# Optimization experiments

Measured on AMD Instinct MI355X. Metric: run time of the kernel, lower is better.

The kernel has to match this reference:

```python
import jax, jax.numpy as jnp
import numpy as np

EPS = 1e-08


def setup_inputs() -> dict:
    key = jax.random.key(0)
    B, D = 8192, 512
    student_output = jax.random.normal(key, (B, D), dtype=jnp.float32)
    return {"student_output": student_output}


def reference(student_output) -> jnp.ndarray:
    # F.normalize(p=2, dim=-1, eps=EPS): x / max(||x||, eps)
    norm = jnp.linalg.norm(student_output, axis=-1, keepdims=True)
    x = student_output / jnp.maximum(norm, EPS)

    n = x.shape[0]
    # Pairwise inner products; mask the diagonal with -1 (self-match)
    dots = jnp.matmul(x, x.T)  # [B, B]
    idx = jnp.arange(n)
    dots = dots.at[idx, idx].set(-1.0)
    I = jnp.argmax(dots, axis=1)  # nearest neighbor index per row

    # torch.nn.PairwiseDistance(2, eps): ||x1 - x2 + eps||_2
    diff = x - x[I] + EPS
    distances = jnp.linalg.norm(diff, axis=-1)  # [B]
    loss = -jnp.mean(jnp.log(distances + EPS))
    return loss
```

## Files before the change

kernel.cpp:

```cpp
#include <hip/hip_runtime.h>
#include <hip/hip_bf16.h>
#include <math.h>

#define D_DIM 512
#define TM    128
#define TN    256

typedef int i32x4 __attribute__((ext_vector_type(4)));
typedef unsigned long long u64;


__device__ inline void async16(unsigned char* lds, const unsigned char* g) {
    __builtin_amdgcn_global_load_lds(
        (const __attribute__((address_space(1))) void*)g,
        (__attribute__((address_space(3))) void*)lds,
        16, 0, 0);
}

__device__ inline bool decode_tile(int l, int& bi, int& bj) {
    const int x    = l & 7;
    const int rank = l >> 3;
    if (rank >= 132) return false;
    const int L0 = 2 * x + 2;
    if (rank < L0)              { bj = x;      bi = rank; }
    else if (rank < 66)         { bj = 31 - x; bi = rank - L0; }
    else if (rank < 2 * x + 84) { bj = x + 8;  bi = rank - 66; }
    else                        { bj = 23 - x; bi = rank - (2 * x + 84); }
    return true;
}


__global__ __launch_bounds__(256) void normalize_rows(
        const float* __restrict__ in, unsigned char* __restrict__ xb,
        float* __restrict__ inv_norm, u64* __restrict__ best,
        float* __restrict__ acc, int* __restrict__ cnt) {
    const int row  = blockIdx.x * 4 + (threadIdx.x >> 6);
    const int lane = threadIdx.x & 63;
    if (blockIdx.x == 0 && threadIdx.x == 0) { acc[0] = 0.f; cnt[0] = 0; }
    const float4* rp = (const float4*)(in + (size_t)row * D_DIM) + lane * 2;
    float4 a = rp[0], b = rp[1];
    float s = a.x*a.x + a.y*a.y + a.z*a.z + a.w*a.w
            + b.x*b.x + b.y*b.y + b.z*b.z + b.w*b.w;
    #pragma unroll
    for (int m = 1; m <= 32; m <<= 1) s += __shfl_xor(s, m, 64);
    float inv = 1.0f / fmaxf(sqrtf(s), 1e-8f);
    if (lane == 0) {
        inv_norm[row] = inv;
        best[row] = 0ull;
    }
    float sc = inv * 127.0f;
    int q0 = __float2int_rn(a.x*sc), q1 = __float2int_rn(a.y*sc);
    int q2 = __float2int_rn(a.z*sc), q3 = __float2int_rn(a.w*sc);
    int q4 = __float2int_rn(b.x*sc), q5 = __float2int_rn(b.y*sc);
    int q6 = __float2int_rn(b.z*sc), q7 = __float2int_rn(b.w*sc);
    int lo = (q0 & 255) | ((q1 & 255) << 8) | ((q2 & 255) << 16) | ((q3 & 255) << 24);
    int hi = (q4 & 255) | ((q5 & 255) << 8) | ((q6 & 255) << 16) | ((q7 & 255) << 24);
    ((int2*)(xb + (size_t)row * D_DIM))[lane] = make_int2(lo, hi);
}


__global__ __launch_bounds__(512, 4) void gemm_argmax(
        const unsigned char* __restrict__ X, u64* __restrict__ best) {
    __shared__ unsigned char smem[73728];
    __shared__ unsigned ready[8];
    __shared__ unsigned readdone[8];
    unsigned char* As0 = smem;
    unsigned char* Bs0 = smem + 24576;
    unsigned int* rmerge = (unsigned int*)smem;
    unsigned int* cmerge = (unsigned int*)(smem + 2048);

    int bi, bj;
    if (!decode_tile(blockIdx.x, bi, bj)) return;
    const int m0 = bi * TM;
    const int n0 = bj * TN;

    const int t    = threadIdx.x;
    const int lane = t & 63;
    const int w    = t >> 6;
    const int wm   = w >> 2;
    const int wn   = w & 3;
    const int qr   = lane & 15;
    const int quad = lane >> 4;

    const int srcsl = ((t & 3) ^ ((t >> 3) & 3)) * 16;
    const unsigned char* gA  = X + (size_t)(m0 + (t >> 2)) * D_DIM + srcsl;
    const unsigned char* gB  = X + (size_t)(n0 + (t >> 2)) * D_DIM + srcsl;
    const unsigned char* gB2 = gB + (size_t)128 * D_DIM;

    if (t < 8)  ready[t] = 0;
    if (t >= 8 && t < 16) readdone[t - 8] = 0;
    __syncthreads();

    i32x4 accm[4][4];
    #pragma unroll
    for (int mi = 0; mi < 4; mi++)
        #pragma unroll
        for (int ni = 0; ni < 4; ni++)
            accm[mi][ni] = (i32x4){0, 0, 0, 0};

    const int rdsl = (quad ^ ((qr >> 1) & 3)) * 16;

    #define STAGE(buf, k0)                                            \
        do {                                                          \
            async16(As0 + (buf) * 8192 + t * 16,         gA + (k0));  \
            async16(Bs0 + (buf) * 16384 + t * 16,        gB + (k0));  \
            async16(Bs0 + (buf) * 16384 + 8192 + t * 16, gB2 + (k0)); \
        } while (0)

    #define SPIN(p, v)                                                \
        while (*(volatile unsigned*)(p) < (v)) __builtin_amdgcn_s_sleep(2)

    STAGE(0, 0);
    STAGE(1, 64);

    #pragma unroll
    for (int t8 = 0; t8 < 8; t8++) {
        const int cur = t8 % 3;
        if (t8 >= 1 && t8 < 6) SPIN(&readdone[t8 - 1], 8u);
        if (t8 < 6) STAGE((t8 + 2) % 3, (t8 + 2) * 64);
        if (t8 < 6)      { asm volatile("s_waitcnt vmcnt(6)" ::: "memory"); }
        else if (t8 == 6){ asm volatile("s_waitcnt vmcnt(3)" ::: "memory"); }
        else             { asm volatile("s_waitcnt vmcnt(0)" ::: "memory"); }
        if (lane == 0) atomicAdd(&ready[t8], 1u);
        SPIN(&ready[t8], 8u);

        i32x4 av[4], bv[4];
        const unsigned char* pA = As0 + cur * 8192  + (wm * 64 + qr) * 64 + rdsl;
        const unsigned char* pB = Bs0 + cur * 16384 + (wn * 64 + qr) * 64 + rdsl;
        #pragma unroll
        for (int mi = 0; mi < 4; mi++)
            av[mi] = *(const i32x4*)(pA + mi * 1024);
        #pragma unroll
        for (int ni = 0; ni < 4; ni++)
            bv[ni] = *(const i32x4*)(pB + ni * 1024);
        asm volatile("s_waitcnt lgkmcnt(0)" ::: "memory");
        if (lane == 0) atomicAdd(&readdone[t8], 1u);

        #pragma unroll
        for (int mi = 0; mi < 4; mi++)
            #pragma unroll
            for (int ni = 0; ni < 4; ni++)
                accm[mi][ni] = __builtin_amdgcn_mfma_i32_16x16x64_i8(
                    av[mi], bv[ni], accm[mi][ni], 0, 0, 0);
    }
    #undef STAGE
    #undef SPIN

    const int colg_base = n0 + wn * 64 + qr;

    #pragma unroll
    for (int mi = 0; mi < 4; mi++) {
        #pragma unroll
        for (int r = 0; r < 4; r++) {
            const int rowl = wm * 64 + mi * 16 + quad * 4 + r;
            const int rowg = m0 + rowl;
            unsigned key = 0u;
            #pragma unroll
            for (int ni = 0; ni < 4; ni++) {
                const int colg = colg_base + ni * 16;
                const unsigned lcol = (unsigned)(wn * 64 + ni * 16 + qr);
                unsigned k = (((unsigned)accm[mi][ni][r] + 0x800000u) << 8)
                           | (255u - lcol);
                k = (colg == rowg) ? 0u : k;
                key = key > k ? key : k;
            }
            #pragma unroll
            for (int m = 1; m <= 8; m <<= 1) {
                unsigned o = (unsigned)__shfl_xor((int)key, m, 64);
                key = key > o ? key : o;
            }
            if (qr == 0) rmerge[rowl * 4 + wn] = key;
        }
    }

    #pragma unroll
    for (int ni = 0; ni < 4; ni++) {
        const int colg = colg_base + ni * 16;
        unsigned key = 0u;
        #pragma unroll
        for (int mi = 0; mi < 4; mi++) {
            #pragma unroll
            for (int r = 0; r < 4; r++) {
                const unsigned lrow = (unsigned)(wm * 64 + mi * 16 + quad * 4 + r);
                const int rowg = m0 + (int)lrow;
                unsigned k = (((unsigned)accm[mi][ni][r] + 0x800000u) << 8)
                           | (255u - lrow);
                k = (rowg == colg) ? 0u : k;
                key = key > k ? key : k;
            }
        }
        unsigned o = (unsigned)__shfl_xor((int)key, 16, 64);
        key = key > o ? key : o;
        o = (unsigned)__shfl_xor((int)key, 32, 64);
        key = key > o ? key : o;
        if (quad == 0) cmerge[(wn * 64 + ni * 16 + qr) * 2 + wm] = key;
    }
    __syncthreads();

    if (t < TM) {
        unsigned a0 = rmerge[t * 4], a1 = rmerge[t * 4 + 1];
        unsigned a2 = rmerge[t * 4 + 2], a3 = rmerge[t * 4 + 3];
        unsigned k01 = a0 > a1 ? a0 : a1;
        unsigned k23 = a2 > a3 ? a2 : a3;
        unsigned k = k01 > k23 ? k01 : k23;
        unsigned bd32 = (k >> 8) + 0x7F800000u;
        unsigned colg = (unsigned)(n0 + 255) - (k & 255u);
        u64 kk = ((u64)bd32 << 32) | (u64)(0xFFFFFFFFu - colg);
        atomicMax(&best[m0 + t], kk);
    }
    if (t < TN) {
        unsigned c0 = cmerge[t * 2], c1 = cmerge[t * 2 + 1];
        unsigned k = c0 > c1 ? c0 : c1;
        unsigned bd32 = (k >> 8) + 0x7F800000u;
        unsigned rowg = (unsigned)(m0 + 255) - (k & 255u);
        u64 kk = ((u64)bd32 << 32) | (u64)(0xFFFFFFFFu - rowg);
        atomicMax(&best[n0 + t], kk);
    }
}


__global__ __launch_bounds__(256) void neighbor_reduce(
        const float* __restrict__ in, const float* __restrict__ inv_norm,
        const u64* __restrict__ best, float* __restrict__ acc,
        int* __restrict__ cnt, float* __restrict__ out, int B) {
    const int wave = threadIdx.x >> 6;
    const int lane = threadIdx.x & 63;
    float lsum = 0.f;
    #pragma unroll
    for (int rr = 0; rr < 8; rr++) {
        const int row = blockIdx.x * 32 + wave * 8 + rr;
        u64 k   = best[row];
        int nbr = (int)(0xFFFFFFFFu - (unsigned)(k & 0xFFFFFFFFull));
        float ir  = inv_norm[row];
        float inb = inv_norm[nbr];
        const float4* rp = (const float4*)(in + (size_t)row * D_DIM) + lane * 2;
        const float4* np = (const float4*)(in + (size_t)nbr * D_DIM) + lane * 2;
        float4 r0 = rp[0], r1 = rp[1], q0 = np[0], q1 = np[1];
        float d0 = r0.x*ir - q0.x*inb + 1e-8f, d1 = r0.y*ir - q0.y*inb + 1e-8f;
        float d2 = r0.z*ir - q0.z*inb + 1e-8f, d3 = r0.w*ir - q0.w*inb + 1e-8f;
        float d4 = r1.x*ir - q1.x*inb + 1e-8f, d5 = r1.y*ir - q1.y*inb + 1e-8f;
        float d6 = r1.z*ir - q1.z*inb + 1e-8f, d7 = r1.w*ir - q1.w*inb + 1e-8f;
        float s = d0*d0 + d1*d1 + d2*d2 + d3*d3 + d4*d4 + d5*d5 + d6*d6 + d7*d7;
        #pragma unroll
        for (int m = 1; m <= 32; m <<= 1) s += __shfl_xor(s, m, 64);
        if (lane == 0) lsum += logf(sqrtf(s) + 1e-8f);
    }
    __shared__ float sb[4];
    if (lane == 0) sb[wave] = lsum;
    __syncthreads();
    if (threadIdx.x == 0) {
        float partial = sb[0] + sb[1] + sb[2] + sb[3];
        atomicAdd(acc, partial);
        __threadfence();
        int done = atomicAdd(cnt, 1);
        if (done == gridDim.x - 1) {
            __threadfence();
            float tot = atomicAdd(acc, 0.0f);
            out[0] = -tot / (float)B;
        }
    }
}


extern "C" void kernel_launch(void* const* d_in, const int* in_sizes, int n_in,
                              void* d_out, int out_size, void* d_ws, size_t ws_size,
                              hipStream_t stream) {
    const float* in = (const float*)d_in[0];
    const int B = in_sizes[0] / D_DIM;
    const int nblk = 144 * 8;

    char* w = (char*)d_ws;
    unsigned char* xb = (unsigned char*)w;
    float* invn = (float*)(w + (size_t)B * D_DIM);
    u64*   best = (u64*)(w + (size_t)B * D_DIM + (size_t)B * 4);
    float* acc  = (float*)(w + (size_t)B * D_DIM + (size_t)B * 4 + (size_t)B * 8);
    int*   cnt  = (int*)(acc + 1);
    float* out  = (float*)d_out;

    normalize_rows<<<B / 4, 256, 0, stream>>>(in, xb, invn, best, acc, cnt);
    gemm_argmax<<<nblk, 512, 0, stream>>>(xb, best);
    neighbor_reduce<<<B / 32, 256, 0, stream>>>(in, invn, best, acc, cnt, out, B);
}
```

Baseline: 113.2 us.

## Replace triple-buffered spin-synced pipeline with single-buffer barrier loop for higher occupancy

Drops the three-stage LDS ring buffer and its atomic-counter spin synchronization in favor of a single staging buffer guarded by __syncthreads each K step. The launch bound is raised to allow more resident blocks per CU, relying on inter-block occupancy instead of intra-block prefetch to hide global load latency. This removes the spin-wait overhead and reduces LDS footprint. It loses load/compute overlap within a block, and there is no explicit vmcnt wait before the barrier, so correctness depends on the compiler inserting one.

```diff
diff --git a/kernel.cpp b/kernel.cpp
--- a/kernel.cpp
+++ b/kernel.cpp
@@ -59,15 +59,12 @@
 }
 
 
-__global__ __launch_bounds__(512, 4) void gemm_argmax(
+__global__ __launch_bounds__(512, 8) void gemm_argmax(
         const unsigned char* __restrict__ X, u64* __restrict__ best) {
-    __shared__ unsigned char smem[73728];
-    __shared__ unsigned ready[8];
-    __shared__ unsigned readdone[8];
-    unsigned char* As0 = smem;
-    unsigned char* Bs0 = smem + 24576;
-    unsigned int* rmerge = (unsigned int*)smem;
-    unsigned int* cmerge = (unsigned int*)(smem + 2048);
+    __shared__ unsigned char As[8192];
+    __shared__ unsigned char Bs[16384];
+    __shared__ unsigned int rmerge[TM * 4];
+    __shared__ unsigned int cmerge[TN * 2];
 
     int bi, bj;
     if (!decode_tile(blockIdx.x, bi, bj)) return;
@@ -87,10 +84,6 @@
     const unsigned char* gB  = X + (size_t)(n0 + (t >> 2)) * D_DIM + srcsl;
     const unsigned char* gB2 = gB + (size_t)128 * D_DIM;
 
-    if (t < 8)  ready[t] = 0;
-    if (t >= 8 && t < 16) readdone[t - 8] = 0;
-    __syncthreads();
-
     i32x4 accm[4][4];
     #pragma unroll
     for (int mi = 0; mi < 4; mi++)
@@ -100,51 +93,32 @@
 
     const int rdsl = (quad ^ ((qr >> 1) & 3)) * 16;
 
-    #define STAGE(buf, k0)                                            \
-        do {                                                          \
-            async16(As0 + (buf) * 8192 + t * 16,         gA + (k0));  \
-            async16(Bs0 + (buf) * 16384 + t * 16,        gB + (k0));  \
-            async16(Bs0 + (buf) * 16384 + 8192 + t * 16, gB2 + (k0)); \
-        } while (0)
-
-    #define SPIN(p, v)                                                \
-        while (*(volatile unsigned*)(p) < (v)) __builtin_amdgcn_s_sleep(2)
-
-    STAGE(0, 0);
-    STAGE(1, 64);
-
-    #pragma unroll
-    for (int t8 = 0; t8 < 8; t8++) {
-        const int cur = t8 % 3;
-        if (t8 >= 1 && t8 < 6) SPIN(&readdone[t8 - 1], 8u);
-        if (t8 < 6) STAGE((t8 + 2) % 3, (t8 + 2) * 64);
-        if (t8 < 6)      { asm volatile("s_waitcnt vmcnt(6)" ::: "memory"); }
-        else if (t8 == 6){ asm volatile("s_waitcnt vmcnt(3)" ::: "memory"); }
-        else             { asm volatile("s_waitcnt vmcnt(0)" ::: "memory"); }
-        if (lane == 0) atomicAdd(&ready[t8], 1u);
-        SPIN(&ready[t8], 8u);
+    #pragma unroll
+    for (int kt = 0; kt < 8; kt++) {
+        const int k0 = kt * 64;
+        async16(As + t * 16,        gA + k0);
+        async16(Bs + t * 16,        gB + k0);
+        async16(Bs + 8192 + t * 16, gB2 + k0);
+        __syncthreads();
 
         i32x4 av[4], bv[4];
-        const unsigned char* pA = As0 + cur * 8192  + (wm * 64 + qr) * 64 + rdsl;
-        const unsigned char* pB = Bs0 + cur * 16384 + (wn * 64 + qr) * 64 + rdsl;
+        const unsigned char* pA = As + (wm * 64 + qr) * 64 + rdsl;
+        const unsigned char* pB = Bs + (wn * 64 + qr) * 64 + rdsl;
         #pragma unroll
         for (int mi = 0; mi < 4; mi++)
             av[mi] = *(const i32x4*)(pA + mi * 1024);
         #pragma unroll
         for (int ni = 0; ni < 4; ni++)
             bv[ni] = *(const i32x4*)(pB + ni * 1024);
-        asm volatile("s_waitcnt lgkmcnt(0)" ::: "memory");
-        if (lane == 0) atomicAdd(&readdone[t8], 1u);
-
         #pragma unroll
         for (int mi = 0; mi < 4; mi++)
             #pragma unroll
             for (int ni = 0; ni < 4; ni++)
                 accm[mi][ni] = __builtin_amdgcn_mfma_i32_16x16x64_i8(
                     av[mi], bv[ni], accm[mi][ni], 0, 0, 0);
-    }
-    #undef STAGE
-    #undef SPIN
+
+        __syncthreads();
+    }
 
     const int colg_base = n0 + wn * 64 + qr;
 
```

Measured after the change: 330.3 us. +191.9%, slower.
